# Optimization experiments

Hardware: AMD Instinct MI355X
Metric: run time of the kernel (lower is better)

## Reference

```python
import jax, jax.numpy as jnp
import numpy as np

Z = 64
P = Z * Z
H = 4  # hDim_1 = hDim_2 = 2*iDim with iDim=2
EPS = 1e-5
WVAR = 0.1  # WEIGHT_VARIANCE stand-in


def setup_inputs() -> dict:
    key = jax.random.key(0)
    ks = jax.random.split(key, 8)
    B = 4096
    x = jax.random.normal(ks[0], (B, Z), dtype=jnp.float32)
    W1 = jax.random.normal(ks[1], (P, 2, H), dtype=jnp.float32) * WVAR
    b1 = jax.random.normal(ks[2], (P, H), dtype=jnp.float32) * WVAR
    g1 = jnp.ones((P, H), dtype=jnp.float32)
    be1 = jnp.zeros((P, H), dtype=jnp.float32)
    W2 = jax.random.normal(ks[3], (P, H, H), dtype=jnp.float32) * WVAR
    b2 = jax.random.normal(ks[4], (P, H), dtype=jnp.float32) * WVAR
    g2 = jnp.ones((P, H), dtype=jnp.float32)
    be2 = jnp.zeros((P, H), dtype=jnp.float32)
    W3 = jax.random.normal(ks[5], (P, H), dtype=jnp.float32) * WVAR
    b3 = jax.random.normal(ks[6], (P,), dtype=jnp.float32) * WVAR
    return {"x": x, "W1": W1, "b1": b1, "g1": g1, "be1": be1,
            "W2": W2, "b2": b2, "g2": g2, "be2": be2,
            "W3": W3, "b3": b3, "dtPt": B}


def _layernorm(h, g, b):
    # LayerNorm over last dim (size H), biased variance, eps=1e-5 (torch default)
    m = jnp.mean(h, axis=-1, keepdims=True)
    v = jnp.mean(jnp.square(h - m), axis=-1, keepdims=True)
    return (h - m) * jax.lax.rsqrt(v + EPS) * g + b


def reference(x, W1, b1, g1, be1, W2, b2, g2, be2, W3, b3, dtPt):
    B = x.shape[0]
    # pairs[b, z*Z+zp] = (x[b,z], x[b,zp])  -> [B, P, 2]
    a = jnp.broadcast_to(x[:, :, None], (B, Z, Z)).reshape(B, P)
    c = jnp.broadcast_to(x[:, None, :], (B, Z, Z)).reshape(B, P)
    pair = jnp.stack([a, c], axis=-1)  # [B, P, 2]
    h = jnp.einsum('bpi,pih->bph', pair, W1) + b1
    h = _layernorm(jnp.tanh(h), g1, be1)
    h = jnp.einsum('bph,phk->bpk', h, W2) + b2
    h = _layernorm(jnp.tanh(h), g2, be2)
    out = jnp.einsum('bph,ph->bp', h, W3) + b3
    out = jax.nn.sigmoid(out)
    return out.reshape(B, Z, Z)
```

## Files before the change

kernel.cpp:

```cpp
#include <hip/hip_runtime.h>
#include <cstddef>

#define ZDIM 64
#define PDIM 4096
#define PB   256
#define BCHUNK 16
#define NPAIR (BCHUNK/2)

typedef float v2f __attribute__((ext_vector_type(2)));

__device__ __forceinline__ v2f pkfma(v2f a, v2f b, v2f c) {
    return __builtin_elementwise_fma(a, b, c);
}
__device__ __forceinline__ v2f splat(float s) { v2f r; r.x = s; r.y = s; return r; }

__device__ __forceinline__ v2f tanh2(v2f x) {
    v2f t = x * x;
    v2f np = t + splat(378.0f);
    np = pkfma(np, t, splat(17325.0f));
    np = pkfma(np, t, splat(135135.0f));
    v2f dp = pkfma(splat(28.0f), t, splat(3150.0f));
    dp = pkfma(dp, t, splat(62370.0f));
    dp = pkfma(dp, t, splat(135135.0f));
    v2f num = x * np;
    v2f r; r.x = __builtin_amdgcn_rcpf(dp.x); r.y = __builtin_amdgcn_rcpf(dp.y);
    return num * r;
}

__global__ void __launch_bounds__(PB, 3) pair_mlp_kernel(
    const float* __restrict__ x,
    const float* __restrict__ W1, const float* __restrict__ b1,
    const float* __restrict__ g1, const float* __restrict__ be1,
    const float* __restrict__ W2, const float* __restrict__ b2,
    const float* __restrict__ g2, const float* __restrict__ be2,
    const float* __restrict__ W3, const float* __restrict__ b3,
    float* __restrict__ out, int nbc)
{
    const int tid = threadIdx.x;
    const int pb  = blockIdx.x / nbc;
    const int bc  = blockIdx.x - pb * nbc;
    const int p   = pb * PB + tid;
    const int z   = __builtin_amdgcn_readfirstlane(p >> 6);
    const int zp  = p & 63;
    const int b0  = bc * BCHUNK;

    const float* xrow = x + (size_t)b0 * ZDIM;
    float cvr[BCHUNK], avr[BCHUNK];
    #pragma unroll
    for (int r = 0; r < BCHUNK; ++r) {
        cvr[r] = xrow[r * ZDIM + zp];
        avr[r] = xrow[r * ZDIM + z];
    }

    const float4* W1v = reinterpret_cast<const float4*>(W1 + (size_t)p * 8);
    const float4 w1x = W1v[0];
    const float4 w1y = W1v[1];
    const float4 b1v  = reinterpret_cast<const float4*>(b1)[p];
    const float4 g1v  = reinterpret_cast<const float4*>(g1)[p];
    const float4 be1v = reinterpret_cast<const float4*>(be1)[p];
    float w2[4][4];
    {
        const float4* W2v = reinterpret_cast<const float4*>(W2 + (size_t)p * 16);
        #pragma unroll
        for (int i = 0; i < 4; ++i) {
            float4 r = W2v[i];
            w2[i][0] = r.x; w2[i][1] = r.y; w2[i][2] = r.z; w2[i][3] = r.w;
        }
    }
    const float4 b2v  = reinterpret_cast<const float4*>(b2)[p];
    const float4 g2v  = reinterpret_cast<const float4*>(g2)[p];
    const float4 be2v = reinterpret_cast<const float4*>(be2)[p];
    const float4 w3v  = reinterpret_cast<const float4*>(W3)[p];
    const float  b3s  = b3[p];

    const float w1a[4] = {w1x.x, w1x.y, w1x.z, w1x.w};
    const float w1b[4] = {w1y.x, w1y.y, w1y.z, w1y.w};
    const float b1a[4] = {b1v.x, b1v.y, b1v.z, b1v.w};
    const float g1a[4] = {g1v.x, g1v.y, g1v.z, g1v.w};
    const float be1a[4]= {be1v.x, be1v.y, be1v.z, be1v.w};
    const float b2a[4] = {b2v.x, b2v.y, b2v.z, b2v.w};
    const float g2a[4] = {g2v.x, g2v.y, g2v.z, g2v.w};
    const float be2a[4]= {be2v.x, be2v.y, be2v.z, be2v.w};
    const float w3a[4] = {w3v.x, w3v.y, w3v.z, w3v.w};

    float w2g[4][4], b2p[4];
    #pragma unroll
    for (int j = 0; j < 4; ++j) b2p[j] = b2a[j];
    #pragma unroll
    for (int i = 0; i < 4; ++i) {
        #pragma unroll
        for (int j = 0; j < 4; ++j) {
            w2g[i][j] = g1a[i] * w2[i][j];
            b2p[j] = __builtin_fmaf(be1a[i], w2[i][j], b2p[j]);
        }
    }
    float w3g[4], b3p = b3s;
    #pragma unroll
    for (int j = 0; j < 4; ++j) {
        w3g[j] = g2a[j] * w3a[j];
        b3p = __builtin_fmaf(be2a[j], w3a[j], b3p);
    }

    float* obase = out + (size_t)b0 * PDIM + p;

    #pragma unroll
    for (int k = 0; k < NPAIR; ++k) {
        v2f a2, c2;
        a2.x = avr[2 * k]; a2.y = avr[2 * k + 1];
        c2.x = cvr[2 * k]; c2.y = cvr[2 * k + 1];

        v2f t0 = tanh2(pkfma(a2, splat(w1a[0]), pkfma(c2, splat(w1b[0]), splat(b1a[0]))));
        v2f t1 = tanh2(pkfma(a2, splat(w1a[1]), pkfma(c2, splat(w1b[1]), splat(b1a[1]))));
        v2f t2 = tanh2(pkfma(a2, splat(w1a[2]), pkfma(c2, splat(w1b[2]), splat(b1a[2]))));
        v2f t3 = tanh2(pkfma(a2, splat(w1a[3]), pkfma(c2, splat(w1b[3]), splat(b1a[3]))));

        v2f s1 = (t0 + t1) + (t2 + t3);
        v2f s2 = pkfma(t0, t0, pkfma(t1, t1, pkfma(t2, t2, t3 * t3)));
        v2f m  = s1 * 0.25f;
        v2f t1e = pkfma(s2, splat(0.25f), splat(1e-5f));
        v2f var = pkfma(s1 * splat(-0.0625f), s1, t1e);
        v2f rs; rs.x = __builtin_amdgcn_rsqf(var.x); rs.y = __builtin_amdgcn_rsqf(var.y);

        v2f d0 = t0 - m, d1 = t1 - m, d2 = t2 - m, d3 = t3 - m;

        v2f u0, u1, u2, u3;
        {
            v2f acc;
            acc = pkfma(d0, splat(w2g[0][0]), pkfma(d1, splat(w2g[1][0]), pkfma(d2, splat(w2g[2][0]), d3 * splat(w2g[3][0]))));
            u0 = tanh2(pkfma(rs, acc, splat(b2p[0])));
            acc = pkfma(d0, splat(w2g[0][1]), pkfma(d1, splat(w2g[1][1]), pkfma(d2, splat(w2g[2][1]), d3 * splat(w2g[3][1]))));
            u1 = tanh2(pkfma(rs, acc, splat(b2p[1])));
            acc = pkfma(d0, splat(w2g[0][2]), pkfma(d1, splat(w2g[1][2]), pkfma(d2, splat(w2g[2][2]), d3 * splat(w2g[3][2]))));
            u2 = tanh2(pkfma(rs, acc, splat(b2p[2])));
            acc = pkfma(d0, splat(w2g[0][3]), pkfma(d1, splat(w2g[1][3]), pkfma(d2, splat(w2g[2][3]), d3 * splat(w2g[3][3]))));
            u3 = tanh2(pkfma(rs, acc, splat(b2p[3])));
        }

        v2f q1 = (u0 + u1) + (u2 + u3);
        v2f q2 = pkfma(u0, u0, pkfma(u1, u1, pkfma(u2, u2, u3 * u3)));
        v2f m2  = q1 * 0.25f;
        v2f t2e = pkfma(q2, splat(0.25f), splat(1e-5f));
        v2f var2 = pkfma(q1 * splat(-0.0625f), q1, t2e);
        v2f rs2; rs2.x = __builtin_amdgcn_rsqf(var2.x); rs2.y = __builtin_amdgcn_rsqf(var2.y);

        v2f e0 = u0 - m2, e1 = u1 - m2, e2 = u2 - m2, e3 = u3 - m2;

        v2f acc3 = pkfma(e0, splat(w3g[0]), pkfma(e1, splat(w3g[1]), pkfma(e2, splat(w3g[2]), e3 * splat(w3g[3]))));
        v2f sarg = pkfma(rs2, acc3, splat(b3p));

        v2f q = sarg * splat(-1.4426950408889634f);
        v2f e; e.x = __builtin_amdgcn_exp2f(q.x); e.y = __builtin_amdgcn_exp2f(q.y);
        v2f ep1 = e + splat(1.0f);

        obase[(size_t)(2 * k) * PDIM]     = __builtin_amdgcn_rcpf(ep1.x);
        obase[(size_t)(2 * k + 1) * PDIM] = __builtin_amdgcn_rcpf(ep1.y);
    }
}

extern "C" void kernel_launch(void* const* d_in, const int* in_sizes, int n_in,
                              void* d_out, int out_size, void* d_ws, size_t ws_size,
                              hipStream_t stream) {
    const float* x   = (const float*)d_in[0];
    const float* W1  = (const float*)d_in[1];
    const float* b1  = (const float*)d_in[2];
    const float* g1  = (const float*)d_in[3];
    const float* be1 = (const float*)d_in[4];
    const float* W2  = (const float*)d_in[5];
    const float* b2  = (const float*)d_in[6];
    const float* g2  = (const float*)d_in[7];
    const float* be2 = (const float*)d_in[8];
    const float* W3  = (const float*)d_in[9];
    const float* b3  = (const float*)d_in[10];
    float* out = (float*)d_out;

    const int B   = in_sizes[0] / ZDIM;
    const int nbc = B / BCHUNK;
    const int grid = (PDIM / PB) * nbc;

    hipLaunchKernelGGL(pair_mlp_kernel, dim3(grid), dim3(PB), 0, stream,
                       x, W1, b1, g1, be1, W2, b2, g2, be2, W3, b3, out, nbc);
}
```

Measured before the change: 137.4 us.

## Use lower-order tanh approximant, stage x row in LDS, two-pass variance

Replaces the [7/6] Padé tanh with a cheaper [5/4] Padé approximant. It also stages the block's x rows in shared memory and reads the c operand from LDS instead of keeping 16 per-thread registers. LayerNorm variance switches to a centred two-pass form, and the launch_bounds occupancy hint is removed. Together these cut ALU work and register pressure, but the lower-order tanh loses accuracy for larger inputs and the change adds a barrier.

```diff
diff --git a/kernel.cpp b/kernel.cpp
--- a/kernel.cpp
+++ b/kernel.cpp
@@ -14,20 +14,15 @@
 }
 __device__ __forceinline__ v2f splat(float s) { v2f r; r.x = s; r.y = s; return r; }
 
-__device__ __forceinline__ v2f tanh2(v2f x) {
+__device__ __forceinline__ v2f tanh54(v2f x) {
     v2f t = x * x;
-    v2f np = t + splat(378.0f);
-    np = pkfma(np, t, splat(17325.0f));
-    np = pkfma(np, t, splat(135135.0f));
-    v2f dp = pkfma(splat(28.0f), t, splat(3150.0f));
-    dp = pkfma(dp, t, splat(62370.0f));
-    dp = pkfma(dp, t, splat(135135.0f));
-    v2f num = x * np;
-    v2f r; r.x = __builtin_amdgcn_rcpf(dp.x); r.y = __builtin_amdgcn_rcpf(dp.y);
+    v2f num = x * pkfma(t, t + splat(105.0f), splat(945.0f));
+    v2f den = pkfma(pkfma(splat(15.0f), t, splat(420.0f)), t, splat(945.0f));
+    v2f r; r.x = __builtin_amdgcn_rcpf(den.x); r.y = __builtin_amdgcn_rcpf(den.y);
     return num * r;
 }
 
-__global__ void __launch_bounds__(PB, 3) pair_mlp_kernel(
+__global__ void __launch_bounds__(PB) pair_mlp_kernel(
     const float* __restrict__ x,
     const float* __restrict__ W1, const float* __restrict__ b1,
     const float* __restrict__ g1, const float* __restrict__ be1,
@@ -44,13 +39,17 @@
     const int zp  = p & 63;
     const int b0  = bc * BCHUNK;
 
+    __shared__ float xs[BCHUNK * ZDIM];
+    {
+        const float4* xg = reinterpret_cast<const float4*>(x + (size_t)b0 * ZDIM);
+        reinterpret_cast<float4*>(xs)[tid] = xg[tid];
+    }
+
     const float* xrow = x + (size_t)b0 * ZDIM;
-    float cvr[BCHUNK], avr[BCHUNK];
+    float avr[BCHUNK];
     #pragma unroll
-    for (int r = 0; r < BCHUNK; ++r) {
-        cvr[r] = xrow[r * ZDIM + zp];
+    for (int r = 0; r < BCHUNK; ++r)
         avr[r] = xrow[r * ZDIM + z];
-    }
 
     const float4* W1v = reinterpret_cast<const float4*>(W1 + (size_t)p * 8);
     const float4 w1x = W1v[0];
@@ -103,51 +102,46 @@
 
     float* obase = out + (size_t)b0 * PDIM + p;
 
+    __syncthreads();
+
     #pragma unroll
     for (int k = 0; k < NPAIR; ++k) {
         v2f a2, c2;
         a2.x = avr[2 * k]; a2.y = avr[2 * k + 1];
-        c2.x = cvr[2 * k]; c2.y = cvr[2 * k + 1];
+        c2.x = xs[(2 * k) * ZDIM + zp];
+        c2.y = xs[(2 * k + 1) * ZDIM + zp];
 
-        v2f t0 = tanh2(pkfma(a2, splat(w1a[0]), pkfma(c2, splat(w1b[0]), splat(b1a[0]))));
-        v2f t1 = tanh2(pkfma(a2, splat(w1a[1]), pkfma(c2, splat(w1b[1]), splat(b1a[1]))));
-        v2f t2 = tanh2(pkfma(a2, splat(w1a[2]), pkfma(c2, splat(w1b[2]), splat(b1a[2]))));
-        v2f t3 = tanh2(pkfma(a2, splat(w1a[3]), pkfma(c2, splat(w1b[3]), splat(b1a[3]))));
+        v2f t0 = tanh54(pkfma(a2, splat(w1a[0]), pkfma(c2, splat(w1b[0]), splat(b1a[0]))));
+        v2f t1 = tanh54(pkfma(a2, splat(w1a[1]), pkfma(c2, splat(w1b[1]), splat(b1a[1]))));
+        v2f t2 = tanh54(pkfma(a2, splat(w1a[2]), pkfma(c2, splat(w1b[2]), splat(b1a[2]))));
+        v2f t3 = tanh54(pkfma(a2, splat(w1a[3]), pkfma(c2, splat(w1b[3]), splat(b1a[3]))));
 
         v2f s1 = (t0 + t1) + (t2 + t3);
-        v2f s2 = pkfma(t0, t0, pkfma(t1, t1, pkfma(t2, t2, t3 * t3)));
         v2f m  = s1 * 0.25f;
-        v2f t1e = pkfma(s2, splat(0.25f), splat(1e-5f));
-        v2f var = pkfma(s1 * splat(-0.0625f), s1, t1e);
+        v2f d0 = t0 - m, d1 = t1 - m, d2 = t2 - m, d3 = t3 - m;
+        v2f sd = pkfma(d0, d0, pkfma(d1, d1, pkfma(d2, d2, d3 * d3)));
+        v2f var = pkfma(sd, splat(0.25f), splat(1e-5f));
         v2f rs; rs.x = __builtin_amdgcn_rsqf(var.x); rs.y = __builtin_amdgcn_rsqf(var.y);
 
-        v2f d0 = t0 - m, d1 = t1 - m, d2 = t2 - m, d3 = t3 - m;
-
-        v2f u0, u1, u2, u3;
-        {
-            v2f acc;
-            acc = pkfma(d0, splat(w2g[0][0]), pkfma(d1, splat(w2g[1][0]), pkfma(d2, splat(w2g[2][0]), d3 * splat(w2g[3][0]))));
-            u0 = tanh2(pkfma(rs, acc, splat(b2p[0])));
-            acc = pkfma(d0, splat(w2g[0][1]), pkfma(d1, splat(w2g[1][1]), pkfma(d2, splat(w2g[2][1]), d3 * splat(w2g[3][1]))));
-            u1 = tanh2(pkfma(rs, acc, splat(b2p[1])));
-            acc = pkfma(d0, splat(w2g[0][2]), pkfma(d1, splat(w2g[1][2]), pkfma(d2, splat(w2g[2][2]), d3 * splat(w2g[3][2]))));
-            u2 = tanh2(pkfma(rs, acc, splat(b2p[2])));
-            acc = pkfma(d0, splat(w2g[0][3]), pkfma(d1, splat(w2g[1][3]), pkfma(d2, splat(w2g[2][3]), d3 * splat(w2g[3][3]))));
-            u3 = tanh2(pkfma(rs, acc, splat(b2p[3])));
-        }
+        v2f acc;
+        acc = pkfma(d0, splat(w2g[0][0]), pkfma(d1, splat(w2g[1][0]), pkfma(d2, splat(w2g[2][0]), d3 * splat(w2g[3][0]))));
+        v2f u0 = tanh54(pkfma(rs, acc, splat(b2p[0])));
+        acc = pkfma(d0, splat(w2g[0][1]), pkfma(d1, splat(w2g[1][1]), pkfma(d2, splat(w2g[2][1]), d3 * splat(w2g[3][1]))));
+        v2f u1 = tanh54(pkfma(rs, acc, splat(b2p[1])));
+        acc = pkfma(d0, splat(w2g[0][2]), pkfma(d1, splat(w2g[1][2]), pkfma(d2, splat(w2g[2][2]), d3 * splat(w2g[3][2]))));
+        v2f u2 = tanh54(pkfma(rs, acc, splat(b2p[2])));
+        acc = pkfma(d0, splat(w2g[0][3]), pkfma(d1, splat(w2g[1][3]), pkfma(d2, splat(w2g[2][3]), d3 * splat(w2g[3][3]))));
+        v2f u3 = tanh54(pkfma(rs, acc, splat(b2p[3])));
 
         v2f q1 = (u0 + u1) + (u2 + u3);
-        v2f q2 = pkfma(u0, u0, pkfma(u1, u1, pkfma(u2, u2, u3 * u3)));
-        v2f m2  = q1 * 0.25f;
-        v2f t2e = pkfma(q2, splat(0.25f), splat(1e-5f));
-        v2f var2 = pkfma(q1 * splat(-0.0625f), q1, t2e);
+        v2f m2 = q1 * 0.25f;
+        v2f e0 = u0 - m2, e1 = u1 - m2, e2 = u2 - m2, e3 = u3 - m2;
+        v2f se = pkfma(e0, e0, pkfma(e1, e1, pkfma(e2, e2, e3 * e3)));
+        v2f var2 = pkfma(se, splat(0.25f), splat(1e-5f));
         v2f rs2; rs2.x = __builtin_amdgcn_rsqf(var2.x); rs2.y = __builtin_amdgcn_rsqf(var2.y);
-
-        v2f e0 = u0 - m2, e1 = u1 - m2, e2 = u2 - m2, e3 = u3 - m2;
 
         v2f acc3 = pkfma(e0, splat(w3g[0]), pkfma(e1, splat(w3g[1]), pkfma(e2, splat(w3g[2]), e3 * splat(w3g[3]))));
         v2f sarg = pkfma(rs2, acc3, splat(b3p));
-
         v2f q = sarg * splat(-1.4426950408889634f);
         v2f e; e.x = __builtin_amdgcn_exp2f(q.x); e.y = __builtin_amdgcn_exp2f(q.y);
         v2f ep1 = e + splat(1.0f);
```

Result: faster. 130.7 us (-4.9%).
